# Performance work log

Hardware: AMD Instinct MI355X
Metric: run time of the kernel (lower is better)

The kernel has to match this reference:

```python
import jax, jax.numpy as jnp
import numpy as np

B, S, D, H = 2, 2048, 768, 12
HD = D // H


def setup_inputs() -> dict:
    key = jax.random.key(0)
    ks = jax.random.split(key, 11)
    scale = 1.0 / np.sqrt(D)
    return {
        "query": jax.random.normal(ks[0], (B, S, D), jnp.float32),
        "key_": jax.random.normal(ks[1], (B, S, D), jnp.float32),
        "value": jax.random.normal(ks[2], (B, S, D), jnp.float32),
        "Wq": jax.random.normal(ks[3], (D, D), jnp.float32) * scale,
        "bq": jnp.zeros((D,), jnp.float32),
        "Wk": jax.random.normal(ks[4], (D, D), jnp.float32) * scale,
        "bk": jnp.zeros((D,), jnp.float32),
        "Wv": jax.random.normal(ks[5], (D, D), jnp.float32) * scale,
        "bv": jnp.zeros((D,), jnp.float32),
        "Wo": jax.random.normal(ks[6], (D, D), jnp.float32) * scale,
        "bo": jnp.zeros((D,), jnp.float32),
    }


def reference(query, key_, value, Wq, bq, Wk, bk, Wv, bv, Wo, bo):
    # Linear projections (W stored as [in, out]); dropout = identity (eval)
    def split_heads(x):
        # [B, S, D] -> [B, H, S, HD]
        return x.reshape(B, S, H, HD).transpose(0, 2, 1, 3)

    Q = split_heads(query @ Wq + bq)
    K = split_heads(key_ @ Wk + bk)
    V = split_heads(value @ Wv + bv)

    inv_sqrt_dk = 1.0 / jnp.sqrt(jnp.asarray(HD, Q.dtype))
    score = jnp.einsum("bhqd,bhkd->bhqk", Q, K) * inv_sqrt_dk  # [B,H,S,S]
    prob = jax.nn.softmax(score, axis=-1)  # source bug: mask is never applied
    out = jnp.einsum("bhqk,bhkd->bhqd", prob, V)  # [B,H,S,HD]
    out = out.transpose(0, 2, 1, 3).reshape(B, S, D)
    return out @ Wo + bo
```

## Files before the change

### kernel.cpp

```cpp
#include <hip/hip_runtime.h>
#include <hip/hip_bf16.h>

#define BB 2
#define SS 2048
#define DDIM 768
#define NH 12
#define HD 64
#define MTOT (BB*SS)

constexpr float QSCALE = 0.125f * 1.44269504088896340736f;

typedef __bf16 bf16_t;
typedef __bf16 bf16x8 __attribute__((ext_vector_type(8)));
typedef __bf16 bf16x4 __attribute__((ext_vector_type(4)));
typedef float  f32x4  __attribute__((ext_vector_type(4)));

static __device__ __forceinline__ f32x4 mfma16(bf16x8 a, bf16x8 b, f32x4 c) {
    return __builtin_amdgcn_mfma_f32_16x16x32_bf16(a, b, c, 0, 0, 0);
}

typedef __attribute__((address_space(3))) unsigned int lds_u32;
typedef __attribute__((address_space(1))) const unsigned int glob_u32;
static __device__ __forceinline__ void gload16(const bf16_t* g, bf16_t* l) {
    __builtin_amdgcn_global_load_lds((glob_u32*)g, (lds_u32*)l, 16, 0, 0);
}

__global__ __launch_bounds__(256) void prep_w(
    const float* __restrict__ Wq, const float* __restrict__ Wk,
    const float* __restrict__ Wv, const float* __restrict__ Wo,
    bf16_t* __restrict__ Wt)
{
    const int z = blockIdx.z, tid = threadIdx.x;
    __shared__ float tile[32][33];
    const float* W = (z == 0) ? Wq : (z == 1) ? Wk : (z == 2) ? Wv : Wo;
    int n0 = blockIdx.x * 32, k0 = blockIdx.y * 32;
    int tx = tid & 31, ty = tid >> 5;
#pragma unroll
    for (int i = 0; i < 4; i++) {
        int k = ty + i * 8;
        tile[k][tx] = W[(size_t)(k0 + k) * DDIM + n0 + tx];
    }
    __syncthreads();
    bf16_t* out = Wt + (size_t)z * DDIM * DDIM;
#pragma unroll
    for (int i = 0; i < 4; i++) {
        int n = ty + i * 8;
        out[(size_t)(n0 + n) * DDIM + k0 + tx] = (bf16_t)tile[tx][n];
    }
}

__global__ __launch_bounds__(256) void gemm_qkv(
    const float* __restrict__ qf32, const float* __restrict__ kf32,
    const float* __restrict__ vf,
    const float* __restrict__ bq, const float* __restrict__ bk, const float* __restrict__ bv,
    const bf16_t* __restrict__ Wt,
    bf16_t* __restrict__ Q, bf16_t* __restrict__ K, bf16_t* __restrict__ Vtg)
{
    __shared__ alignas(16) bf16_t As[64 * 64];
    __shared__ alignas(16) bf16_t Bs[128 * 64];
    const int gid = blockIdx.x;
    const int lid = (gid & 7) * 144 + (gid >> 3);
    const int z   = lid / 384;
    const int rem = lid - z * 384;
    const int mi  = rem / 6, ni = rem - mi * 6;
    const int m0 = mi * 64, n0 = ni * 128;

    const int tid = threadIdx.x, lane = tid & 63, w = tid >> 6;
    const int wm = (w >> 1) * 32, wn = (w & 1) * 64;
    const int quad = lane >> 4, l15 = lane & 15;

    const float* Af = (z == 0) ? qf32 : (z == 1) ? kf32 : vf;
    const bf16_t* Bt = Wt + (size_t)z * (DDIM * DDIM);
    const int arow = lane >> 3;
    const int asl  = ((lane & 7) ^ arow) * 8;
    bf16_t* BsW = &Bs[w * 2048];
    const int frow = tid >> 2, fq = tid & 3;
    const int rsw = frow & 7;
    const float* Abase = Af + (size_t)(m0 + frow) * DDIM + fq * 16;

    f32x4 acc[2][4];
#pragma unroll
    for (int mt = 0; mt < 2; mt++)
#pragma unroll
        for (int nt = 0; nt < 4; nt++) { f32x4 zz = {0.f,0.f,0.f,0.f}; acc[mt][nt] = zz; }

    f32x4 vA[4];
#pragma unroll
    for (int i = 0; i < 4; i++) vA[i] = *(const f32x4*)(Abase + 4 * i);

    for (int k0 = 0; k0 < DDIM; k0 += 64) {
        __syncthreads();
#pragma unroll
        for (int j = 0; j < 2; j++) {
            bf16x8 oj;
#pragma unroll
            for (int e = 0; e < 4; e++) {
                oj[e]     = (bf16_t)vA[2 * j][e];
                oj[e + 4] = (bf16_t)vA[2 * j + 1][e];
            }
            int phys = (fq * 2 + j) ^ rsw;
            *(bf16x8*)&As[frow * 64 + phys * 8] = oj;
        }
        {
            const bf16_t* Bg = Bt + (size_t)(n0 + w * 32 + arow) * DDIM + k0 + asl;
#pragma unroll
            for (int i = 0; i < 4; i++)
                gload16(Bg + (size_t)(8 * i) * DDIM, BsW + 512 * i);
        }
        __syncthreads();
        if (k0 + 64 < DDIM) {
            const float* nsrc = Abase + k0 + 64;
#pragma unroll
            for (int i = 0; i < 4; i++) vA[i] = *(const f32x4*)(nsrc + 4 * i);
        }
#pragma unroll
        for (int h = 0; h < 2; h++) {
            bf16x8 a[2], b[4];
#pragma unroll
            for (int mt = 0; mt < 2; mt++) {
                int r = wm + mt * 16 + l15;
                a[mt] = *(const bf16x8*)&As[r * 64 + (((h * 4 + quad) ^ (r & 7)) * 8)];
            }
#pragma unroll
            for (int nt = 0; nt < 4; nt++) {
                int r = wn + nt * 16 + l15;
                b[nt] = *(const bf16x8*)&Bs[r * 64 + (((h * 4 + quad) ^ (r & 7)) * 8)];
            }
#pragma unroll
            for (int mt = 0; mt < 2; mt++)
#pragma unroll
                for (int nt = 0; nt < 4; nt++)
                    acc[mt][nt] = mfma16(a[mt], b[nt], acc[mt][nt]);
        }
    }

    const float* bias = (z == 0) ? bq : (z == 1) ? bk : bv;
    float bvals[4];
#pragma unroll
    for (int nt = 0; nt < 4; nt++)
        bvals[nt] = bias[n0 + wn + nt * 16 + l15];

    if (z == 2) {
#pragma unroll
        for (int mt = 0; mt < 2; mt++) {
            int row0 = m0 + wm + mt * 16 + quad * 4;
#pragma unroll
            for (int nt = 0; nt < 4; nt++) {
                int col = n0 + wn + nt * 16 + l15;
                bf16x4 pk;
#pragma unroll
                for (int r = 0; r < 4; r++) pk[r] = (bf16_t)(acc[mt][nt][r] + bvals[nt]);
                *(bf16x4*)&Vtg[(size_t)col * MTOT + row0] = pk;
            }
        }
    } else {
        bf16_t* C = (z == 0) ? Q : K;
        float scale = (z == 0) ? QSCALE : 1.0f;
#pragma unroll
        for (int mt = 0; mt < 2; mt++) {
            int row0 = m0 + wm + mt * 16 + quad * 4;
#pragma unroll
            for (int nt = 0; nt < 4; nt++) {
                int col = n0 + wn + nt * 16 + l15;
#pragma unroll
                for (int r = 0; r < 4; r++)
                    C[(size_t)(row0 + r) * DDIM + col] = (bf16_t)((acc[mt][nt][r] + bvals[nt]) * scale);
            }
        }
    }
}

__global__ __launch_bounds__(256) void gemm_out(
    const bf16_t* __restrict__ Ab, const bf16_t* __restrict__ Bt,
    const float* __restrict__ bo, float* __restrict__ out)
{
    __shared__ alignas(16) bf16_t As[64 * 64];
    __shared__ alignas(16) bf16_t Bs[64 * 64];
    const int gid = blockIdx.x;
    const int lid = (gid & 7) * 96 + (gid >> 3);
    const int mi  = lid / 12, ni = lid - mi * 12;
    const int m0 = mi * 64, n0 = ni * 64;

    const int tid = threadIdx.x, lane = tid & 63, w = tid >> 6;
    const int wm = (w >> 1) * 32, wn = (w & 1) * 32;
    const int quad = lane >> 4, l15 = lane & 15;
    const int arow = lane >> 3;
    const int asl  = ((lane & 7) ^ arow) * 8;
    bf16_t* AsW = &As[w * 1024];
    bf16_t* BsW = &Bs[w * 1024];

    f32x4 acc[2][2];
#pragma unroll
    for (int mt = 0; mt < 2; mt++)
#pragma unroll
        for (int nt = 0; nt < 2; nt++) { f32x4 zz = {0.f,0.f,0.f,0.f}; acc[mt][nt] = zz; }

    for (int k0 = 0; k0 < DDIM; k0 += 64) {
        __syncthreads();
        {
            const bf16_t* Ag = Ab + (size_t)(m0 + w * 16 + arow) * DDIM + k0 + asl;
            gload16(Ag, AsW);
            gload16(Ag + (size_t)8 * DDIM, AsW + 512);
            const bf16_t* Bg = Bt + (size_t)(n0 + w * 16 + arow) * DDIM + k0 + asl;
            gload16(Bg, BsW);
            gload16(Bg + (size_t)8 * DDIM, BsW + 512);
        }
        __syncthreads();

#pragma unroll
        for (int h = 0; h < 2; h++) {
            bf16x8 a[2], b[2];
#pragma unroll
            for (int mt = 0; mt < 2; mt++) {
                int r = wm + mt * 16 + l15;
                a[mt] = *(const bf16x8*)&As[r * 64 + (((h * 4 + quad) ^ (r & 7)) * 8)];
            }
#pragma unroll
            for (int nt = 0; nt < 2; nt++) {
                int r = wn + nt * 16 + l15;
                b[nt] = *(const bf16x8*)&Bs[r * 64 + (((h * 4 + quad) ^ (r & 7)) * 8)];
            }
#pragma unroll
            for (int mt = 0; mt < 2; mt++)
#pragma unroll
                for (int nt = 0; nt < 2; nt++)
                    acc[mt][nt] = mfma16(a[mt], b[nt], acc[mt][nt]);
        }
    }

    float bvals[2];
#pragma unroll
    for (int nt = 0; nt < 2; nt++)
        bvals[nt] = bo[n0 + wn + nt * 16 + l15];
#pragma unroll
    for (int mt = 0; mt < 2; mt++) {
        int row0 = m0 + wm + mt * 16 + quad * 4;
#pragma unroll
        for (int nt = 0; nt < 2; nt++) {
            int col = n0 + wn + nt * 16 + l15;
#pragma unroll
            for (int r = 0; r < 4; r++)
                out[(size_t)(row0 + r) * DDIM + col] = acc[mt][nt][r] + bvals[nt];
        }
    }
}

__global__ __launch_bounds__(256) void attn_kernel(
    const bf16_t* __restrict__ Qb, const bf16_t* __restrict__ Kb,
    const bf16_t* __restrict__ Vtg, bf16_t* __restrict__ Ab)
{
    const int id = blockIdx.x;
    const int hb = id % 24, qi = id / 24;
    const int h = hb % NH, b = hb / NH;
    const int q0 = qi * 64;
    const int tid = threadIdx.x, lane = tid & 63, w = tid >> 6;
    const int quad = lane >> 4, l15 = lane & 15;

    __shared__ union {
        struct {
            alignas(16) bf16_t Ps[2][64][144];
        } a;
        struct {
            alignas(16) float Obuf[2][64][68];
            float Lb[4][64];
        } m;
    } u;

    bf16x8 qf[4][2];
#pragma unroll
    for (int qt = 0; qt < 4; qt++) {
        const bf16_t* src = Qb + (size_t)(b * SS + q0 + qt * 16 + l15) * DDIM + h * HD;
#pragma unroll
        for (int kh = 0; kh < 2; kh++)
            qf[qt][kh] = *(const bf16x8*)(src + kh * 32 + quad * 8);
    }

    f32x4 o[4][4];
#pragma unroll
    for (int dt = 0; dt < 4; dt++)
#pragma unroll
        for (int qt = 0; qt < 4; qt++) { f32x4 z = {0.f,0.f,0.f,0.f}; o[dt][qt] = z; }
    float l_s[4];
#pragma unroll
    for (int qt = 0; qt < 4; qt++) l_s[qt] = 0.f;

    const bf16_t* kfrag = Kb + (size_t)(b * SS + w * 32 + l15) * DDIM + h * HD + quad * 8;
    const bf16_t* vfrag = Vtg + (size_t)(h * HD + l15) * MTOT + b * SS + w * 32 + quad * 8;

#pragma unroll 2
    for (int kt0 = 0; kt0 < SS; kt0 += 128) {
        const int pb = (kt0 >> 7) & 1;
        f32x4 s_[2][4];
#pragma unroll
        for (int kt = 0; kt < 2; kt++) {
            const bf16_t* kr = kfrag + (size_t)(kt0 + kt * 16) * DDIM;
            bf16x8 ak0 = *(const bf16x8*)(kr);
            bf16x8 ak1 = *(const bf16x8*)(kr + 32);
#pragma unroll
            for (int qt = 0; qt < 4; qt++) {
                f32x4 z = {0.f,0.f,0.f,0.f};
                z = mfma16(ak0, qf[qt][0], z);
                z = mfma16(ak1, qf[qt][1], z);
                s_[kt][qt] = z;
            }
        }

#pragma unroll
        for (int qt = 0; qt < 4; qt++) {
            float rs = l_s[qt];
#pragma unroll
            for (int kt = 0; kt < 2; kt++) {
                bf16x4 pk;
#pragma unroll
                for (int r = 0; r < 4; r++) {
                    float p = __builtin_amdgcn_exp2f(s_[kt][qt][r]);
                    rs += p;
                    pk[r] = (bf16_t)p;
                }
                *(bf16x4*)&u.a.Ps[pb][qt * 16 + l15][w * 32 + kt * 16 + quad * 4] = pk;
            }
            l_s[qt] = rs;
        }

        bf16x8 av8[4], bp[4];
#pragma unroll
        for (int dt = 0; dt < 4; dt++)
            av8[dt] = *(const bf16x8*)(vfrag + (size_t)(dt * 16) * MTOT + kt0);
#pragma unroll
        for (int qt = 0; qt < 4; qt++)
            bp[qt] = *(const bf16x8*)&u.a.Ps[pb][qt * 16 + l15][w * 32 + quad * 8];
#pragma unroll
        for (int dt = 0; dt < 4; dt++)
#pragma unroll
            for (int qt = 0; qt < 4; qt++)
                o[dt][qt] = mfma16(av8[dt], bp[qt], o[dt][qt]);
    }

#pragma unroll
    for (int qt = 0; qt < 4; qt++) {
        float rs = l_s[qt];
        rs += __shfl_xor(rs, 16, 64);
        rs += __shfl_xor(rs, 32, 64);
        l_s[qt] = rs;
    }
    __syncthreads();
    if (quad == 0) {
#pragma unroll
        for (int qt = 0; qt < 4; qt++)
            u.m.Lb[w][qt * 16 + l15] = l_s[qt];
    }
    __syncthreads();
    float lstar[4];
#pragma unroll
    for (int qt = 0; qt < 4; qt++) {
        int q = qt * 16 + l15;
        lstar[qt] = u.m.Lb[0][q] + u.m.Lb[1][q] + u.m.Lb[2][q] + u.m.Lb[3][q];
    }
    if (w >= 2) {
        float* dst = &u.m.Obuf[w - 2][lane][0];
#pragma unroll
        for (int dt = 0; dt < 4; dt++)
#pragma unroll
            for (int qt = 0; qt < 4; qt++)
                *(f32x4*)(dst + (dt * 4 + qt) * 4) = o[dt][qt];
    }
    __syncthreads();
    if (w < 2) {
        const float* src = &u.m.Obuf[w][lane][0];
#pragma unroll
        for (int dt = 0; dt < 4; dt++)
#pragma unroll
            for (int qt = 0; qt < 4; qt++)
                o[dt][qt] += *(const f32x4*)(src + (dt * 4 + qt) * 4);
    }
    __syncthreads();
    if (w == 1) {
        float* dst = &u.m.Obuf[0][lane][0];
#pragma unroll
        for (int dt = 0; dt < 4; dt++)
#pragma unroll
            for (int qt = 0; qt < 4; qt++)
                *(f32x4*)(dst + (dt * 4 + qt) * 4) = o[dt][qt];
    }
    __syncthreads();
    if (w == 0) {
        const float* src = &u.m.Obuf[0][lane][0];
#pragma unroll
        for (int dt = 0; dt < 4; dt++)
#pragma unroll
            for (int qt = 0; qt < 4; qt++)
                o[dt][qt] += *(const f32x4*)(src + (dt * 4 + qt) * 4);
#pragma unroll
        for (int qt = 0; qt < 4; qt++) {
            float inv = 1.f / lstar[qt];
            size_t rbase = (size_t)(b * SS + q0 + qt * 16 + l15) * DDIM + h * HD;
#pragma unroll
            for (int dt = 0; dt < 4; dt++) {
                bf16x4 pk;
#pragma unroll
                for (int r = 0; r < 4; r++) pk[r] = (bf16_t)(o[dt][qt][r] * inv);
                *(bf16x4*)&Ab[rbase + dt * 16 + quad * 4] = pk;
            }
        }
    }
}

extern "C" void kernel_launch(void* const* d_in, const int* in_sizes, int n_in,
                              void* d_out, int out_size, void* d_ws, size_t ws_size,
                              hipStream_t stream)
{
    const float* q  = (const float*)d_in[0];
    const float* k  = (const float*)d_in[1];
    const float* v  = (const float*)d_in[2];
    const float* Wq = (const float*)d_in[3];
    const float* bq = (const float*)d_in[4];
    const float* Wk = (const float*)d_in[5];
    const float* bk = (const float*)d_in[6];
    const float* Wv = (const float*)d_in[7];
    const float* bv = (const float*)d_in[8];
    const float* Wo = (const float*)d_in[9];
    const float* bo = (const float*)d_in[10];
    float* out = (float*)d_out;

    bf16_t* Wt  = (bf16_t*)d_ws;
    bf16_t* Ab  = Wt + (size_t)4 * DDIM * DDIM;
    bf16_t* Qs  = Ab + (size_t)MTOT * DDIM;
    bf16_t* Ks  = Qs + (size_t)MTOT * DDIM;
    bf16_t* Vtg = Ks + (size_t)MTOT * DDIM;

    prep_w<<<dim3(24, 24, 4), 256, 0, stream>>>(Wq, Wk, Wv, Wo, Wt);
    gemm_qkv<<<dim3(1152), 256, 0, stream>>>(q, k, v, bq, bk, bv, Wt, Qs, Ks, Vtg);
    attn_kernel<<<dim3((SS / 64) * NH * BB), 256, 0, stream>>>(Qs, Ks, Vtg, Ab);
    gemm_out<<<dim3(768), 256, 0, stream>>>(Ab, Wt + (size_t)3 * DDIM * DDIM, bo, out);
}
```

Baseline: 207.7 us.

## Split attention key range across two wave groups with 512-thread blocks

```diff
diff --git a/kernel.cpp b/kernel.cpp
--- a/kernel.cpp
+++ b/kernel.cpp
@@ -245,7 +245,7 @@
     }
 }
 
-__global__ __launch_bounds__(256) void attn_kernel(
+__global__ __launch_bounds__(512) void attn_kernel(
     const bf16_t* __restrict__ Qb, const bf16_t* __restrict__ Kb,
     const bf16_t* __restrict__ Vtg, bf16_t* __restrict__ Ab)
 {
@@ -254,6 +254,7 @@
     const int h = hb % NH, b = hb / NH;
     const int q0 = qi * 64;
     const int tid = threadIdx.x, lane = tid & 63, w = tid >> 6;
+    const int g = w >> 2, wv = w & 3;
     const int quad = lane >> 4, l15 = lane & 15;
 
     __shared__ union {
@@ -262,7 +263,7 @@
         } a;
         struct {
             alignas(16) float Obuf[2][64][68];
-            float Lb[4][64];
+            float Lb[8][64];
         } m;
     } u;
 
@@ -284,12 +285,11 @@
 #pragma unroll
     for (int qt = 0; qt < 4; qt++) l_s[qt] = 0.f;
 
-    const bf16_t* kfrag = Kb + (size_t)(b * SS + w * 32 + l15) * DDIM + h * HD + quad * 8;
-    const bf16_t* vfrag = Vtg + (size_t)(h * HD + l15) * MTOT + b * SS + w * 32 + quad * 8;
-
-#pragma unroll 2
-    for (int kt0 = 0; kt0 < SS; kt0 += 128) {
-        const int pb = (kt0 >> 7) & 1;
+    const int kbase = g * 1024;
+    const bf16_t* kfrag = Kb + (size_t)(b * SS + kbase + wv * 32 + l15) * DDIM + h * HD + quad * 8;
+    const bf16_t* vfrag = Vtg + (size_t)(h * HD + l15) * MTOT + b * SS + kbase + wv * 32 + quad * 8;
+
+    for (int kt0 = 0; kt0 < 1024; kt0 += 128) {
         f32x4 s_[2][4];
 #pragma unroll
         for (int kt = 0; kt < 2; kt++) {
@@ -317,7 +317,7 @@
                     rs += p;
                     pk[r] = (bf16_t)p;
                 }
-                *(bf16x4*)&u.a.Ps[pb][qt * 16 + l15][w * 32 + kt * 16 + quad * 4] = pk;
+                *(bf16x4*)&u.a.Ps[g][qt * 16 + l15][wv * 32 + kt * 16 + quad * 4] = pk;
             }
             l_s[qt] = rs;
         }
@@ -328,7 +328,7 @@
             av8[dt] = *(const bf16x8*)(vfrag + (size_t)(dt * 16) * MTOT + kt0);
 #pragma unroll
         for (int qt = 0; qt < 4; qt++)
-            bp[qt] = *(const bf16x8*)&u.a.Ps[pb][qt * 16 + l15][w * 32 + quad * 8];
+            bp[qt] = *(const bf16x8*)&u.a.Ps[g][qt * 16 + l15][wv * 32 + quad * 8];
 #pragma unroll
         for (int dt = 0; dt < 4; dt++)
 #pragma unroll
@@ -354,9 +354,12 @@
 #pragma unroll
     for (int qt = 0; qt < 4; qt++) {
         int q = qt * 16 + l15;
-        lstar[qt] = u.m.Lb[0][q] + u.m.Lb[1][q] + u.m.Lb[2][q] + u.m.Lb[3][q];
-    }
-    if (w >= 2) {
+        float s0 = u.m.Lb[0][q] + u.m.Lb[1][q] + u.m.Lb[2][q] + u.m.Lb[3][q];
+        float s1 = u.m.Lb[4][q] + u.m.Lb[5][q] + u.m.Lb[6][q] + u.m.Lb[7][q];
+        lstar[qt] = s0 + s1;
+    }
+
+    if (w == 2 || w == 3) {
         float* dst = &u.m.Obuf[w - 2][lane][0];
 #pragma unroll
         for (int dt = 0; dt < 4; dt++)
@@ -365,7 +368,7 @@
                 *(f32x4*)(dst + (dt * 4 + qt) * 4) = o[dt][qt];
     }
     __syncthreads();
-    if (w < 2) {
+    if (w == 0 || w == 1) {
         const float* src = &u.m.Obuf[w][lane][0];
 #pragma unroll
         for (int dt = 0; dt < 4; dt++)
@@ -374,7 +377,43 @@
                 o[dt][qt] += *(const f32x4*)(src + (dt * 4 + qt) * 4);
     }
     __syncthreads();
-    if (w == 1) {
+    if (w == 6 || w == 7) {
+        float* dst = &u.m.Obuf[w - 6][lane][0];
+#pragma unroll
+        for (int dt = 0; dt < 4; dt++)
+#pragma unroll
+            for (int qt = 0; qt < 4; qt++)
+                *(f32x4*)(dst + (dt * 4 + qt) * 4) = o[dt][qt];
+    }
+    __syncthreads();
+    if (w == 4 || w == 5) {
+        const float* src = &u.m.Obuf[w - 4][lane][0];
+#pragma unroll
+        for (int dt = 0; dt < 4; dt++)
+#pragma unroll
+            for (int qt = 0; qt < 4; qt++)
+                o[dt][qt] += *(const f32x4*)(src + (dt * 4 + qt) * 4);
+    }
+    __syncthreads();
+    if (w == 1 || w == 5) {
+        float* dst = &u.m.Obuf[w == 1 ? 0 : 1][lane][0];
+#pragma unroll
+        for (int dt = 0; dt < 4; dt++)
+#pragma unroll
+            for (int qt = 0; qt < 4; qt++)
+                *(f32x4*)(dst + (dt * 4 + qt) * 4) = o[dt][qt];
+    }
+    __syncthreads();
+    if (w == 0 || w == 4) {
+        const float* src = &u.m.Obuf[w == 0 ? 0 : 1][lane][0];
+#pragma unroll
+        for (int dt = 0; dt < 4; dt++)
+#pragma unroll
+            for (int qt = 0; qt < 4; qt++)
+                o[dt][qt] += *(const f32x4*)(src + (dt * 4 + qt) * 4);
+    }
+    __syncthreads();
+    if (w == 4) {
         float* dst = &u.m.Obuf[0][lane][0];
 #pragma unroll
         for (int dt = 0; dt < 4; dt++)
@@ -430,6 +469,6 @@
 
     prep_w<<<dim3(24, 24, 4), 256, 0, stream>>>(Wq, Wk, Wv, Wo, Wt);
     gemm_qkv<<<dim3(1152), 256, 0, stream>>>(q, k, v, bq, bk, bv, Wt, Qs, Ks, Vtg);
-    attn_kernel<<<dim3((SS / 64) * NH * BB), 256, 0, stream>>>(Qs, Ks, Vtg, Ab);
+    attn_kernel<<<dim3((SS / 64) * NH * BB), 512, 0, stream>>>(Qs, Ks, Vtg, Ab);
     gemm_out<<<dim3(768), 256, 0, stream>>>(Ab, Wt + (size_t)3 * DDIM * DDIM, bo, out);
 }
```

New measurement: 205.5 us. About the same (-1.0%).
